# Kernel tuning notes

Hardware: AMD Instinct MI355X
Metric: run time of the kernel (lower is better)

Reference implementation:

```python
import jax, jax.numpy as jnp
import numpy as np

B, N, E = 8, 64, 192
D_IN, D_PROJ = 1024, 256
F = 16            # cfg.NGM.GNN_FEAT per layer
SK_TAU = 0.05     # cfg.NGM.SK_TAU
SK_ITERS = 10
BIN_ITERS = 10
NN = N * N


def _project(x, Wp, bp, gamma, beta):
    # self.projection: Linear(1024,256) -> BatchNorm1d(256) (batch stats) -> ReLU
    B_, M, _ = x.shape
    h = x.reshape(B_ * M, -1) @ Wp + bp
    mu = h.mean(0)
    var = h.var(0)
    h = (h - mu) / jnp.sqrt(var + 1e-5) * gamma + beta
    return jax.nn.relu(h).reshape(B_, M, -1)


def _l2n(x):
    return x / jnp.clip(jnp.linalg.norm(x, axis=-1, keepdims=True), 1e-12)


def _log_sinkhorn(log_s, iters):
    for _ in range(iters):
        log_s = log_s - jax.nn.logsumexp(log_s, axis=2, keepdims=True)
        log_s = log_s - jax.nn.logsumexp(log_s, axis=1, keepdims=True)
    return jnp.exp(log_s)


def _build_K(Ke, Kp, s1, d1, s2, d2):
    # construct_sparse_aff_mat: K[a2*N+a1, b2*N+b1] += Ke[e1, e2]
    rows = s2[None, :] * N + s1[:, None]      # [E, E]
    cols = d2[None, :] * N + d1[:, None]      # [E, E]
    flat = (rows.astype(jnp.int32) * NN + cols.astype(jnp.int32)).ravel()
    K = jnp.zeros((NN * NN,), Ke.dtype).at[flat].add(Ke.ravel()).reshape(NN, NN)
    diag = jnp.arange(NN)
    # diagonal holds vec(Kp^T) (ordering a2*N + a1, matching emb = Kp.T.reshape(-1,1))
    return K.at[diag, diag].set(Kp.T.ravel())


def setup_inputs() -> dict:
    key = jax.random.key(0)
    ks = jax.random.split(key, 32)
    inp = {}
    inp['x1'] = jax.random.normal(ks[0], (B, N, D_IN), jnp.float32)
    inp['x2'] = jax.random.normal(ks[1], (B, N, D_IN), jnp.float32)
    inp['e1'] = jax.random.normal(ks[2], (B, E, D_IN), jnp.float32)
    inp['e2'] = jax.random.normal(ks[3], (B, E, D_IN), jnp.float32)
    inp['Wp'] = jax.random.normal(ks[4], (D_IN, D_PROJ), jnp.float32) * 0.02
    inp['bp'] = jnp.zeros((D_PROJ,), jnp.float32)
    inp['gamma'] = jnp.ones((D_PROJ,), jnp.float32)
    inp['beta'] = jnp.zeros((D_PROJ,), jnp.float32)
    in_dims = [1, F + 1, F + 1]
    for i, din in enumerate(in_dims):
        inp[f'W{i}'] = jax.random.normal(ks[5 + 3 * i], (din, F), jnp.float32) * 0.2
        inp[f'b{i}'] = jnp.zeros((F,), jnp.float32)
        inp[f'S{i}'] = jax.random.normal(ks[6 + 3 * i], (F, 1), jnp.float32) * 0.2
        inp[f'c{i}'] = jnp.zeros((1,), jnp.float32)
    inp['Wc'] = jax.random.normal(ks[20], (F + 1, 1), jnp.float32) * 0.2
    inp['bc'] = jnp.zeros((1,), jnp.float32)
    inp['bin_value'] = jnp.ones((1,), jnp.float32) * 0.2
    inp['src1'] = jax.random.randint(ks[21], (B, E), 0, N, jnp.int32)
    inp['dst1'] = jax.random.randint(ks[22], (B, E), 0, N, jnp.int32)
    inp['src2'] = jax.random.randint(ks[23], (B, E), 0, N, jnp.int32)
    inp['dst2'] = jax.random.randint(ks[24], (B, E), 0, N, jnp.int32)
    return inp


def reference(x1, x2, e1, e2, Wp, bp, gamma, beta,
              W0, b0, S0, c0, W1, b1, S1, c1, W2, b2, S2, c2,
              Wc, bc, bin_value, src1, dst1, src2, dst2):
    # unary / quadratic affinities via projected, L2-normalized inner products
    p1 = _project(x1, Wp, bp, gamma, beta)
    p2 = _project(x2, Wp, bp, gamma, beta)
    q1 = _project(e1, Wp, bp, gamma, beta)
    q2 = _project(e2, Wp, bp, gamma, beta)
    Kp = jnp.einsum('bnd,bmd->bnm', _l2n(p1), _l2n(p2))        # [B, N1, N2]
    Ke = 0.5 * jnp.einsum('bed,bfd->bef', _l2n(q1), _l2n(q2))  # [B, E1, E2]
    # sparse Kronecker affinity assembled densely (association graph adjacency)
    K = jax.vmap(_build_K)(Ke, Kp, src1, dst1, src2, dst2)     # [B, NN, NN]
    A = (K > 0).astype(K.dtype)
    deg = jnp.clip(A.sum(-1), 1.0)                              # [B, NN]
    x = Kp.transpose(0, 2, 1).reshape(B, NN, 1)                 # emb = vec(Kp^T)
    for (W, b, S, c) in ((W0, b0, S0, c0), (W1, b1, S1, c1), (W2, b2, S2, c2)):
        msg = jnp.einsum('bij,bjc->bic', K, x) / deg[..., None]  # sparse matvec (memory-bound)
        h = jax.nn.relu(msg @ W + b)                             # [B, NN, F]
        v = (h @ S + c).reshape(B, N, N)                         # row order a2*N+a1 -> [B, N2, N1]
        ss = _log_sinkhorn(v.transpose(0, 2, 1) / SK_TAU, SK_ITERS)  # Sinkhorn embedding channel
        x = jnp.concatenate([h, ss.transpose(0, 2, 1).reshape(B, NN, 1)], -1)
    v = (x @ Wc + bc).reshape(B, N, N)
    s = v.transpose(0, 2, 1)                                    # [B, N1, N2]
    # BinSinkhorn: pad with learned bin value, dual normalization, strip bin
    binv = bin_value[0]
    ls = jnp.concatenate([s, jnp.full((B, 1, N), binv, s.dtype)], 1)
    ls = jnp.concatenate([ls, jnp.full((B, N + 1, 1), binv, s.dtype)], 2)
    P = _log_sinkhorn(ls, BIN_ITERS)
    ss = P[:, :N, :N]
    return ss / jax.lax.stop_gradient(ss.max())
```

## Files before the change

kernel.cpp:

```cpp
#include <hip/hip_runtime.h>

constexpr int kB   = 8;
constexpr int kN   = 64;
constexpr int kE   = 192;
constexpr int kDin = 1024;
constexpr int kDp  = 256;
constexpr int kNN  = 4096;
constexpr float kTauInv = 20.0f;
constexpr int kXS  = 16;
constexpr int kXP  = 18;

typedef float vfloat4 __attribute__((ext_vector_type(4)));

struct SmemGemm { float As[2][16][68]; float Ws[2][16][68]; };
struct SmemCsr  {
    int km1[4096], km2[4096];
    short es1[kE], es2[kE], rp1[kE], rp2[kE];
    int cnt1[64], cnt2[64], pos1[64], pos2[64];
    int ccnt1[kE], ccnt2[kE], cpos1[kE], cpos2[kE];
};
union __align__(16) SmemK1 { SmemGemm g; SmemCsr csr; };

__global__ __launch_bounds__(256) void k_projcsr(
    const float* __restrict__ x1, const float* __restrict__ x2,
    const float* __restrict__ e1, const float* __restrict__ e2,
    const float* __restrict__ Wp,
    const int* __restrict__ src1, const int* __restrict__ dst1,
    const int* __restrict__ src2, const int* __restrict__ dst2,
    float* __restrict__ P,
    int* __restrict__ off1, int* __restrict__ off2,
    int* __restrict__ lst1, int* __restrict__ lst2,
    int* __restrict__ rep1g, int* __restrict__ rep2g,
    int* __restrict__ coff1, int* __restrict__ coff2,
    int* __restrict__ clst1, int* __restrict__ clst2)
{
    const int bid = blockIdx.x, t = threadIdx.x;
    __shared__ SmemK1 u;

    if (bid < 512) {
        const int z = bid >> 8;
        const int rt = (bid >> 2) & 63, ct = bid & 3;
        const int grow0 = rt * 64, col0 = ct * 64;
        const float* src; int lrow0;
        if (rt < 8)       { src = x1; lrow0 = grow0; }
        else if (rt < 16) { src = x2; lrow0 = grow0 - 512; }
        else if (rt < 40) { src = e1; lrow0 = grow0 - 1024; }
        else              { src = e2; lrow0 = grow0 - 2560; }

        const int tx = t & 15, ty = t >> 4;
        const int arow = t >> 2, acol = (t & 3) * 4;
        const int wrow = t >> 4, wcol = (t & 15) * 4;

        const float* Abase = src + (size_t)(lrow0 + arow) * kDin + z * 512 + acol;
        const float* Wbase = Wp + (size_t)(z * 512 + wrow) * kDp + col0 + wcol;

        float4 a4 = *(const float4*)Abase;
        float4 w4 = *(const float4*)Wbase;
        float acc[4][4] = {};

        for (int c = 0; c < 32; ++c) {
            const int cur = c & 1;
            u.g.As[cur][acol + 0][arow] = a4.x;
            u.g.As[cur][acol + 1][arow] = a4.y;
            u.g.As[cur][acol + 2][arow] = a4.z;
            u.g.As[cur][acol + 3][arow] = a4.w;
            *(float4*)&u.g.Ws[cur][wrow][wcol] = w4;
            __syncthreads();
            if (c < 31) {
                a4 = *(const float4*)(Abase + (c + 1) * 16);
                w4 = *(const float4*)(Wbase + (size_t)(c + 1) * 16 * kDp);
            }
#pragma unroll
            for (int kk = 0; kk < 16; ++kk) {
                float4 av = *(const float4*)&u.g.As[cur][kk][ty * 4];
                float4 wv = *(const float4*)&u.g.Ws[cur][kk][tx * 4];
                float a[4] = {av.x, av.y, av.z, av.w};
                float w[4] = {wv.x, wv.y, wv.z, wv.w};
#pragma unroll
                for (int i = 0; i < 4; ++i)
#pragma unroll
                    for (int j = 0; j < 4; ++j)
                        acc[i][j] += a[i] * w[j];
            }
        }
        float* Pz = P + (size_t)z * 1048576;
#pragma unroll
        for (int i = 0; i < 4; ++i) {
            const int row = grow0 + ty * 4 + i;
            vfloat4 v;
            v.x = acc[i][0]; v.y = acc[i][1]; v.z = acc[i][2]; v.w = acc[i][3];
            __builtin_nontemporal_store(v, (vfloat4*)&Pz[(size_t)row * kDp + col0 + tx * 4]);
        }
    } else {
        const int b = bid - 512;
        auto& C = u.csr;
        for (int i = t; i < 4096; i += 256) {
            C.km1[i] = 0x7fffffff; C.km2[i] = 0x7fffffff;
        }
        if (t < 64) { C.cnt1[t] = 0; C.cnt2[t] = 0; }
        for (int i = t; i < kE; i += 256) { C.ccnt1[i] = 0; C.ccnt2[i] = 0; }
        __syncthreads();
        if (t < kE) {
            int v1 = src1[b * kE + t], v2 = src2[b * kE + t];
            C.es1[t] = (short)v1; C.es2[t] = (short)v2;
            atomicAdd(&C.cnt1[v1], 1);
            atomicAdd(&C.cnt2[v2], 1);
            atomicMin(&C.km1[v1 * 64 + dst1[b * kE + t]], t);
            atomicMin(&C.km2[v2 * 64 + dst2[b * kE + t]], t);
        }
        __syncthreads();
        if (t < kE) {
            int r1 = C.km1[C.es1[t] * 64 + dst1[b * kE + t]];
            int r2 = C.km2[C.es2[t] * 64 + dst2[b * kE + t]];
            C.rp1[t] = (short)r1; C.rp2[t] = (short)r2;
            rep1g[b * kE + t] = r1; rep2g[b * kE + t] = r2;
            atomicAdd(&C.ccnt1[r1], 1);
            atomicAdd(&C.ccnt2[r2], 1);
        }
        __syncthreads();
        if (t == 0) {
            int a = 0, c = 0;
            for (int v = 0; v < 64; ++v) { C.pos1[v] = a; a += C.cnt1[v]; C.pos2[v] = c; c += C.cnt2[v]; }
            a = 0; c = 0;
            for (int v = 0; v < kE; ++v) { C.cpos1[v] = a; a += C.ccnt1[v]; C.cpos2[v] = c; c += C.ccnt2[v]; }
        }
        __syncthreads();
        if (t < 64) { off1[b * 65 + t] = C.pos1[t]; off2[b * 65 + t] = C.pos2[t]; }
        if (t == 0) { off1[b * 65 + 64] = kE; off2[b * 65 + 64] = kE; }
        if (t < kE) { coff1[b * 193 + t] = C.cpos1[t]; coff2[b * 193 + t] = C.cpos2[t]; }
        if (t == 0) { coff1[b * 193 + kE] = kE; coff2[b * 193 + kE] = kE; }
        __syncthreads();
        if (t < kE) {
            int p = atomicAdd(&C.pos1[C.es1[t]], 1); lst1[b * kE + p] = t;
            int q = atomicAdd(&C.pos2[C.es2[t]], 1); lst2[b * kE + q] = t;
            int cp = atomicAdd(&C.cpos1[C.rp1[t]], 1); clst1[b * kE + cp] = t;
            int cq = atomicAdd(&C.cpos2[C.rp2[t]], 1); clst2[b * kE + cq] = t;
        }
    }
}

__global__ __launch_bounds__(256) void k_reduce(
    const float* __restrict__ P, const float* __restrict__ bp,
    float* __restrict__ hbuf, float* __restrict__ stats)
{
    const int t = threadIdx.x;
    const int r0 = blockIdx.x * 16;
    const int seg = (r0 < 512) ? 0 : (r0 < 1024 ? 1 : (r0 < 2560 ? 2 : 3));
    const float bb = bp[t];
    float s = 0.f, s2 = 0.f;
#pragma unroll
    for (int rr = 0; rr < 16; ++rr) {
        size_t o = (size_t)(r0 + rr) * kDp + t;
        float v = P[o] + P[o + 1048576] + bb;
        hbuf[o] = v;
        s += v; s2 += v * v;
    }
    atomicAdd(&stats[seg * 512 + t], s);
    atomicAdd(&stats[seg * 512 + 256 + t], s2);
}

struct __align__(16) SmemSim  {
    float Xs[32][36]; float Ys[32][36];
    float muX[256], isX[256], muY[256], isY[256];
    float ga[256], be[256];
    float scX[32], scY[32];
};

__global__ __launch_bounds__(256) void k_sim(
    const float* __restrict__ hbuf, const float* __restrict__ stats,
    const float* __restrict__ gamma, const float* __restrict__ beta,
    float* __restrict__ Kp, float* __restrict__ Ke)
{
    const int bid = blockIdx.x, t = threadIdx.x;
    __shared__ SmemSim u;

    const int id = bid % 40, b = bid / 40;
    int mt, nt_, ldo, segX, segY, xrow0, yrow0; float* outp; float scale;
    if (id < 4) {
        mt = (id >> 1) * 32; nt_ = (id & 1) * 32; ldo = 64;
        xrow0 = b * 64; yrow0 = 512 + b * 64;
        segX = 0; segY = 1;
        outp = Kp + (size_t)b * 4096; scale = 1.0f;
    } else {
        int e = id - 4;
        mt = (e / 6) * 32; nt_ = (e % 6) * 32; ldo = 192;
        xrow0 = 1024 + b * 192; yrow0 = 2560 + b * 192;
        segX = 2; segY = 3;
        outp = Ke + (size_t)b * 36864; scale = 0.5f;
    }
    {
        const float n = (segX < 2) ? 512.f : 1536.f;
        float mu = stats[segX * 512 + t] / n;
        float var = stats[segX * 512 + 256 + t] / n - mu * mu;
        u.muX[t] = mu; u.isX[t] = rsqrtf(var + 1e-5f);
        mu = stats[segY * 512 + t] / n;
        var = stats[segY * 512 + 256 + t] / n - mu * mu;
        u.muY[t] = mu; u.isY[t] = rsqrtf(var + 1e-5f);
        u.ga[t] = gamma[t]; u.be[t] = beta[t];
    }
    __syncthreads();
    {
        const int ri = t >> 2, lane = t & 3;
        const bool isXr = ri < 32;
        const int grow = isXr ? (xrow0 + mt + ri) : (yrow0 + nt_ + (ri - 32));
        const float* mus = isXr ? u.muX : u.muY;
        const float* iss = isXr ? u.isX : u.isY;
        const float* hr = hbuf + (size_t)grow * kDp;
        float ss = 0.f;
        for (int c4 = 0; c4 < 16; ++c4) {
            int c = lane * 64 + c4 * 4;
            float4 v = *(const float4*)&hr[c];
            float p;
            p = fmaxf((v.x - mus[c+0]) * iss[c+0] * u.ga[c+0] + u.be[c+0], 0.f); ss += p * p;
            p = fmaxf((v.y - mus[c+1]) * iss[c+1] * u.ga[c+1] + u.be[c+1], 0.f); ss += p * p;
            p = fmaxf((v.z - mus[c+2]) * iss[c+2] * u.ga[c+2] + u.be[c+2], 0.f); ss += p * p;
            p = fmaxf((v.w - mus[c+3]) * iss[c+3] * u.ga[c+3] + u.be[c+3], 0.f); ss += p * p;
        }
        ss += __shfl_xor(ss, 1);
        ss += __shfl_xor(ss, 2);
        if (lane == 0) {
            float sc = 1.f / fmaxf(sqrtf(ss), 1e-12f);
            if (isXr) u.scX[ri] = sc; else u.scY[ri - 32] = sc;
        }
    }
    __syncthreads();
    const int row = t >> 3, kq = t & 7;
    const int ty = t >> 4, tx = t & 15;
    const float* Xp = hbuf + (size_t)(xrow0 + mt) * kDp;
    const float* Yp = hbuf + (size_t)(yrow0 + nt_) * kDp;
    float acc[2][2] = {};
    for (int k0 = 0; k0 < kDp; k0 += 32) {
        const int c = k0 + kq * 4;
        float4 xa = *(const float4*)(Xp + (size_t)row * kDp + c);
        float4 ya = *(const float4*)(Yp + (size_t)row * kDp + c);
        const float sx = u.scX[row], sy = u.scY[row];
        u.Xs[kq*4+0][row] = fmaxf((xa.x - u.muX[c+0]) * u.isX[c+0] * u.ga[c+0] + u.be[c+0], 0.f) * sx;
        u.Xs[kq*4+1][row] = fmaxf((xa.y - u.muX[c+1]) * u.isX[c+1] * u.ga[c+1] + u.be[c+1], 0.f) * sx;
        u.Xs[kq*4+2][row] = fmaxf((xa.z - u.muX[c+2]) * u.isX[c+2] * u.ga[c+2] + u.be[c+2], 0.f) * sx;
        u.Xs[kq*4+3][row] = fmaxf((xa.w - u.muX[c+3]) * u.isX[c+3] * u.ga[c+3] + u.be[c+3], 0.f) * sx;
        u.Ys[kq*4+0][row] = fmaxf((ya.x - u.muY[c+0]) * u.isY[c+0] * u.ga[c+0] + u.be[c+0], 0.f) * sy;
        u.Ys[kq*4+1][row] = fmaxf((ya.y - u.muY[c+1]) * u.isY[c+1] * u.ga[c+1] + u.be[c+1], 0.f) * sy;
        u.Ys[kq*4+2][row] = fmaxf((ya.z - u.muY[c+2]) * u.isY[c+2] * u.ga[c+2] + u.be[c+2], 0.f) * sy;
        u.Ys[kq*4+3][row] = fmaxf((ya.w - u.muY[c+3]) * u.isY[c+3] * u.ga[c+3] + u.be[c+3], 0.f) * sy;
        __syncthreads();
#pragma unroll
        for (int kk = 0; kk < 32; ++kk) {
            float2 xv = *(const float2*)&u.Xs[kk][ty * 2];
            float2 yv = *(const float2*)&u.Ys[kk][tx * 2];
            acc[0][0] += xv.x * yv.x; acc[0][1] += xv.x * yv.y;
            acc[1][0] += xv.y * yv.x; acc[1][1] += xv.y * yv.y;
        }
        __syncthreads();
    }
#pragma unroll
    for (int i = 0; i < 2; ++i)
#pragma unroll
        for (int j = 0; j < 2; ++j)
            __builtin_nontemporal_store(scale * acc[i][j],
                &outp[(size_t)(mt + ty * 2 + i) * ldo + nt_ + tx * 2 + j]);
}

struct __align__(16) SmemLayer {
    float mat[64][68]; float fL[64], gL[64];
    float WL[17 * 16]; float bL[16], SL[16]; float c0v;
    float WcL[17];
    int jd2[kE]; int il[kE]; float msgT[64][18];
    int co1L[kE + 1], co2L[kE + 1];
    short cl1L[kE], cl2L[kE];
    float xs[64][kXP];
};

__device__ void sink64_local(int b, int t, float (*mat)[68], float* fL, float* gL,
                             const float* __restrict__ vin)
{
    const float4* v4 = (const float4*)(vin + b * kNN);
    for (int i = t; i < 1024; i += 256) {
        float4 v = v4[i];
        int idx = i * 4;
        int q = idx >> 6, p = idx & 63;
        mat[p][q]     = v.x * kTauInv;
        mat[p + 1][q] = v.y * kTauInv;
        mat[p + 2][q] = v.z * kTauInv;
        mat[p + 3][q] = v.w * kTauInv;
    }
    if (t < 64) { fL[t] = 0.f; gL[t] = 0.f; }
    __syncthreads();
    const int r = t >> 2, s = t & 3;
    float tv[16];
    for (int it = 0; it < 10; ++it) {
        float mx = -1e30f;
#pragma unroll
        for (int k = 0; k < 16; ++k) {
            float v = mat[r][s + 4 * k] + gL[s + 4 * k];
            tv[k] = v; mx = fmaxf(mx, v);
        }
        mx = fmaxf(mx, __shfl_xor(mx, 1));
        mx = fmaxf(mx, __shfl_xor(mx, 2));
        float sum = 0.f;
#pragma unroll
        for (int k = 0; k < 16; ++k) sum += __expf(tv[k] - mx);
        sum += __shfl_xor(sum, 1);
        sum += __shfl_xor(sum, 2);
        if (s == 0) fL[r] = -(mx + __logf(sum));
        __syncthreads();
        mx = -1e30f;
#pragma unroll
        for (int k = 0; k < 16; ++k) {
            float v = mat[s + 4 * k][r] + fL[s + 4 * k];
            tv[k] = v; mx = fmaxf(mx, v);
        }
        mx = fmaxf(mx, __shfl_xor(mx, 1));
        mx = fmaxf(mx, __shfl_xor(mx, 2));
        sum = 0.f;
#pragma unroll
        for (int k = 0; k < 16; ++k) sum += __expf(tv[k] - mx);
        sum += __shfl_xor(sum, 1);
        sum += __shfl_xor(sum, 2);
        if (s == 0) gL[r] = -(mx + __logf(sum));
        __syncthreads();
    }
    const float fr = fL[r];
#pragma unroll
    for (int k = 0; k < 16; ++k) {
        int q = s + 4 * k;
        mat[r][q] = __expf(mat[r][q] + fr + gL[q]);
    }
    __syncthreads();
}

template <int C, bool LASTP>
__device__ void layer_body(int bid, int t, SmemLayer& L,
    const int* __restrict__ off1, const int* __restrict__ lst1,
    const int* __restrict__ off2, const int* __restrict__ lst2,
    const int* __restrict__ d1, const int* __restrict__ d2,
    const int* __restrict__ rep1g, const int* __restrict__ rep2g,
    const int* __restrict__ coff1, const int* __restrict__ coff2,
    const int* __restrict__ clst1, const int* __restrict__ clst2,
    const float* __restrict__ Ke, const float* __restrict__ x,
    const float* __restrict__ Kp, int* __restrict__ degcnt,
    const float* __restrict__ W, const float* __restrict__ bb,
    const float* __restrict__ S, const float* __restrict__ c0,
    const float* __restrict__ Wc,
    const float* __restrict__ vprev, float* __restrict__ xn,
    float* __restrict__ vcbuf, float* __restrict__ vout)
{
    const int r2 = bid & 63, b = bid >> 6;
    for (int k = t; k < C * 16; k += 256) L.WL[k] = W[k];
    if (t < 16) { L.bL[t] = bb[t]; L.SL[t] = S[t]; }
    if (t == 0) L.c0v = c0[0];
    if (LASTP && t < 17) L.WcL[t] = Wc[t];
    const int j0 = off2[b * 65 + r2];
    const int n2 = off2[b * 65 + r2 + 1] - j0;
    for (int k = t; k < n2; k += 256) {
        int j = lst2[b * kE + j0 + k];
        int v = (j << 8) | d2[b * kE + j];
        if (C == 1 && rep2g[b * kE + j] == j) v |= 1 << 16;
        L.jd2[k] = v;
    }
    for (int k = t; k < kE; k += 256) {
        int i = lst1[b * kE + k];
        int v = (i << 8) | d1[b * kE + i];
        if (C == 1 && rep1g[b * kE + i] == i) v |= 1 << 16;
        L.il[k] = v;
    }
    if constexpr (C == 1) {
        for (int k = t; k < kE + 1; k += 256) {
            L.co1L[k] = coff1[b * 193 + k];
            L.co2L[k] = coff2[b * 193 + k];
        }
        for (int k = t; k < kE; k += 256) {
            L.cl1L[k] = (short)clst1[b * kE + k];
            L.cl2L[k] = (short)clst2[b * kE + k];
        }
    }
    if constexpr (C == 17) {
        sink64_local(b, t, L.mat, L.fL, L.gL, vprev);
    } else {
        __syncthreads();
    }

    const int r1 = t >> 2, lane = t & 3;
    const int i0 = off1[b * 65 + r1], i1 = off1[b * 65 + r1 + 1];
    const float* Keb = Ke + (size_t)b * kE * kE;
    const float* KpB = Kp + (size_t)b * kNN;
    int degLocal = 0;

    if constexpr (C == 1) {
        float acc = 0.f;
        for (int k = 0; k < n2; ++k) {
            int pk = L.jd2[k], j = (pk >> 8) & 255, dd2 = pk & 255;
            for (int m = i0 + lane; m < i1; m += 4) {
                int pi = L.il[m], i = (pi >> 8) & 255, dd1 = pi & 255;
                if (dd2 == r2 && dd1 == r1) continue;
                acc += Keb[(size_t)i * kE + j] * KpB[dd1 * 64 + dd2];
            }
        }
        acc += __shfl_xor(acc, 1);
        acc += __shfl_xor(acc, 2);
        if (lane == 0) L.msgT[r1][0] = acc;
        for (int m = i0 + lane; m < i1; m += 4) {
            int pi = L.il[m];
            if (!(pi >> 16)) continue;
            int i = (pi >> 8) & 255, dd1 = pi & 255;
            for (int k = 0; k < n2; ++k) {
                int pk = L.jd2[k];
                if (!(pk >> 16)) continue;
                int j = (pk >> 8) & 255, dd2 = pk & 255;
                float sum = 0.f;
                for (int mm = L.co1L[i]; mm < L.co1L[i + 1]; ++mm) {
                    const float* kr = Keb + (size_t)L.cl1L[mm] * kE;
                    for (int nn = L.co2L[j]; nn < L.co2L[j + 1]; ++nn)
                        sum += kr[L.cl2L[nn]];
                }
                if ((r2 * 64 + r1) != (dd2 * 64 + dd1) && sum > 0.0f) ++degLocal;
            }
        }
        degLocal += __shfl_xor(degLocal, 1);
        degLocal += __shfl_xor(degLocal, 2);
    } else {
        const float* xb = x + (size_t)b * kNN * kXS;
        float acc[5];
#pragma unroll
        for (int cc = 0; cc < 5; ++cc) acc[cc] = 0.f;
        for (int k = 0; k < n2; ++k) {
            int pk = L.jd2[k], j = (pk >> 8) & 255, dd2 = pk & 255;
            __syncthreads();
            {
                const float4* src4 = (const float4*)(xb + (size_t)(dd2 * 64) * kXS);
                float4 vv = src4[t];
                const int row = t >> 2, c4 = (t & 3) * 4;
                L.xs[row][c4 + 0] = vv.x; L.xs[row][c4 + 1] = vv.y;
                L.xs[row][c4 + 2] = vv.z; L.xs[row][c4 + 3] = vv.w;
            }
            __syncthreads();
            for (int m = i0; m < i1; ++m) {
                int pi = L.il[m], dd1 = pi & 255;
                if (dd2 == r2 && dd1 == r1) continue;
                int i = (pi >> 8) & 255;
                float kv = Keb[(size_t)i * kE + j];
                const float* xc = &L.xs[dd1][0];
                acc[0] += kv * xc[lane];
                acc[1] += kv * xc[lane + 4];
                acc[2] += kv * xc[lane + 8];
                acc[3] += kv * xc[lane + 12];
                if (lane == 0) acc[4] += kv * L.mat[dd1][dd2];
            }
        }
#pragma unroll
        for (int cc = 0; cc < 5; ++cc) {
            int c = lane + cc * 4;
            if (c < C) L.msgT[r1][c] = acc[cc];
        }
    }
    __syncthreads();

    const int row = r2 * 64 + r1;
    const int idx = b * kNN + row;
    const float kd = KpB[r1 * 64 + r2];
    int degv;
    if constexpr (C == 1) {
        degv = degLocal;
        if (lane == 0) __builtin_nontemporal_store(degLocal, &degcnt[idx]);
    } else {
        degv = degcnt[idx];
    }
    const float dg = fmaxf((float)(degv + (kd > 0.f ? 1 : 0)), 1.f);
    float m[C];
    if constexpr (C == 1) {
        m[0] = (L.msgT[r1][0] + kd * kd) / dg;
    } else {
        float4 xa  = *(const float4*)(x + (size_t)idx * kXS + 0);
        float4 xb4 = *(const float4*)(x + (size_t)idx * kXS + 4);
        float4 xc4 = *(const float4*)(x + (size_t)idx * kXS + 8);
        float4 xd4 = *(const float4*)(x + (size_t)idx * kXS + 12);
        m[0]  = (L.msgT[r1][0]  + kd * xa.x) / dg;
        m[1]  = (L.msgT[r1][1]  + kd * xa.y) / dg;
        m[2]  = (L.msgT[r1][2]  + kd * xa.z) / dg;
        m[3]  = (L.msgT[r1][3]  + kd * xa.w) / dg;
        m[4]  = (L.msgT[r1][4]  + kd * xb4.x) / dg;
        m[5]  = (L.msgT[r1][5]  + kd * xb4.y) / dg;
        m[6]  = (L.msgT[r1][6]  + kd * xb4.z) / dg;
        m[7]  = (L.msgT[r1][7]  + kd * xb4.w) / dg;
        m[8]  = (L.msgT[r1][8]  + kd * xc4.x) / dg;
        m[9]  = (L.msgT[r1][9]  + kd * xc4.y) / dg;
        m[10] = (L.msgT[r1][10] + kd * xc4.z) / dg;
        m[11] = (L.msgT[r1][11] + kd * xc4.w) / dg;
        m[12] = (L.msgT[r1][12] + kd * xd4.x) / dg;
        m[13] = (L.msgT[r1][13] + kd * xd4.y) / dg;
        m[14] = (L.msgT[r1][14] + kd * xd4.z) / dg;
        m[15] = (L.msgT[r1][15] + kd * xd4.w) / dg;
        m[16] = (L.msgT[r1][16] + kd * L.mat[r1][r2]) / dg;
    }
    float h[4];
    float vpart = 0.f;
#pragma unroll
    for (int ff = 0; ff < 4; ++ff) {
        int f = lane * 4 + ff;
        float a = L.bL[f];
#pragma unroll
        for (int c = 0; c < C; ++c) a += m[c] * L.WL[c * 16 + f];
        h[ff] = fmaxf(a, 0.f);
        vpart += h[ff] * L.SL[f];
    }
    if constexpr (!LASTP) {
        vfloat4 hv; hv.x = h[0]; hv.y = h[1]; hv.z = h[2]; hv.w = h[3];
        __builtin_nontemporal_store(hv, (vfloat4*)(xn + (size_t)idx * kXS + lane * 4));
    } else {
        float vcp = h[0] * L.WcL[lane * 4 + 0] + h[1] * L.WcL[lane * 4 + 1]
                  + h[2] * L.WcL[lane * 4 + 2] + h[3] * L.WcL[lane * 4 + 3];
        vcp += __shfl_xor(vcp, 1);
        vcp += __shfl_xor(vcp, 2);
        if (lane == 0) __builtin_nontemporal_store(vcp, &vcbuf[idx]);
    }
    vpart += __shfl_xor(vpart, 1);
    vpart += __shfl_xor(vpart, 2);
    if (lane == 0) __builtin_nontemporal_store(vpart + L.c0v, &vout[idx]);
}

__global__ __launch_bounds__(256) void k_l0(
    const int* __restrict__ off1, const int* __restrict__ lst1,
    const int* __restrict__ off2, const int* __restrict__ lst2,
    const int* __restrict__ dst1, const int* __restrict__ dst2,
    const int* __restrict__ rep1g, const int* __restrict__ rep2g,
    const int* __restrict__ coff1, const int* __restrict__ coff2,
    const int* __restrict__ clst1, const int* __restrict__ clst2,
    const float* __restrict__ Ke, const float* __restrict__ Kp,
    int* __restrict__ degcnt,
    const float* __restrict__ W0, const float* __restrict__ b0,
    const float* __restrict__ S0, const float* __restrict__ c0,
    float* __restrict__ xA, float* __restrict__ vA)
{
    __shared__ SmemLayer L;
    layer_body<1, false>(blockIdx.x, threadIdx.x, L,
        off1, lst1, off2, lst2, dst1, dst2, rep1g, rep2g,
        coff1, coff2, clst1, clst2, Ke, nullptr, Kp, degcnt,
        W0, b0, S0, c0, nullptr, nullptr, xA, nullptr, vA);
}

__global__ __launch_bounds__(256) void k_l1(
    const int* __restrict__ off1, const int* __restrict__ lst1,
    const int* __restrict__ off2, const int* __restrict__ lst2,
    const int* __restrict__ dst1, const int* __restrict__ dst2,
    const float* __restrict__ Ke, const float* __restrict__ Kp,
    int* __restrict__ degcnt,
    const float* __restrict__ W1, const float* __restrict__ b1,
    const float* __restrict__ S1, const float* __restrict__ c1,
    const float* __restrict__ xA, const float* __restrict__ vA,
    float* __restrict__ xB, float* __restrict__ vB)
{
    __shared__ SmemLayer L;
    layer_body<17, false>(blockIdx.x, threadIdx.x, L,
        off1, lst1, off2, lst2, dst1, dst2, nullptr, nullptr,
        nullptr, nullptr, nullptr, nullptr, Ke, xA, Kp, degcnt,
        W1, b1, S1, c1, nullptr, vA, xB, nullptr, vB);
}

__global__ __launch_bounds__(256) void k_l2(
    const int* __restrict__ off1, const int* __restrict__ lst1,
    const int* __restrict__ off2, const int* __restrict__ lst2,
    const int* __restrict__ dst1, const int* __restrict__ dst2,
    const float* __restrict__ Ke, const float* __restrict__ Kp,
    int* __restrict__ degcnt,
    const float* __restrict__ W2, const float* __restrict__ b2,
    const float* __restrict__ S2, const float* __restrict__ c2,
    const float* __restrict__ Wc,
    const float* __restrict__ xB, const float* __restrict__ vB,
    float* __restrict__ vcbuf, float* __restrict__ vA)
{
    __shared__ SmemLayer L;
    layer_body<17, true>(blockIdx.x, threadIdx.x, L,
        off1, lst1, off2, lst2, dst1, dst2, nullptr, nullptr,
        nullptr, nullptr, nullptr, nullptr, Ke, xB, Kp, degcnt,
        W2, b2, S2, c2, Wc, vB, nullptr, vcbuf, vA);
}

struct __align__(16) SmemSinkF {
    float mat[65][68]; float fL[72], gL[72];
    float wred[9];
};

__global__ __launch_bounds__(576) void k_final(
    const float* __restrict__ vA, const float* __restrict__ vcbuf,
    const float* __restrict__ Wc, const float* __restrict__ bc,
    const float* __restrict__ binv,
    int* __restrict__ bars, float* __restrict__ out)
{
    const int b = blockIdx.x, t = threadIdx.x;
    __shared__ SmemSinkF S;

    for (int i = t; i < kNN; i += 576) {
        int q = i >> 6, p = i & 63;
        S.mat[p][q] = vA[b * kNN + i] * kTauInv;
    }
    if (t < 72) { S.fL[t] = 0.f; S.gL[t] = 0.f; }
    __syncthreads();

    const int r = t >> 3, s = t & 7;

    {
        const bool act = r < 64;
        const int rr = act ? r : 0;
        float Lr[8], Lc[8], tv[8];
#pragma unroll
        for (int k = 0; k < 8; ++k) {
            Lr[k] = S.mat[rr][s + 8 * k];
            Lc[k] = S.mat[s + 8 * k][rr];
        }
        __syncthreads();
        for (int it = 0; it < 10; ++it) {
            float mx = -1e30f;
#pragma unroll
            for (int k = 0; k < 8; ++k) { tv[k] = Lr[k] + S.gL[s + 8 * k]; mx = fmaxf(mx, tv[k]); }
            mx = fmaxf(mx, __shfl_xor(mx, 1));
            mx = fmaxf(mx, __shfl_xor(mx, 2));
            mx = fmaxf(mx, __shfl_xor(mx, 4));
            float sum = 0.f;
#pragma unroll
            for (int k = 0; k < 8; ++k) sum += __expf(tv[k] - mx);
            sum += __shfl_xor(sum, 1);
            sum += __shfl_xor(sum, 2);
            sum += __shfl_xor(sum, 4);
            if (act && s == 0) S.fL[r] = -(mx + __logf(sum));
            __syncthreads();
            mx = -1e30f;
#pragma unroll
            for (int k = 0; k < 8; ++k) { tv[k] = Lc[k] + S.fL[s + 8 * k]; mx = fmaxf(mx, tv[k]); }
            mx = fmaxf(mx, __shfl_xor(mx, 1));
            mx = fmaxf(mx, __shfl_xor(mx, 2));
            mx = fmaxf(mx, __shfl_xor(mx, 4));
            sum = 0.f;
#pragma unroll
            for (int k = 0; k < 8; ++k) sum += __expf(tv[k] - mx);
            sum += __shfl_xor(sum, 1);
            sum += __shfl_xor(sum, 2);
            sum += __shfl_xor(sum, 4);
            if (act && s == 0) S.gL[r] = -(mx + __logf(sum));
            __syncthreads();
        }
        if (act) {
            const float fr = S.fL[r];
#pragma unroll
            for (int k = 0; k < 8; ++k) {
                int q = s + 8 * k;
                S.mat[r][q] = __expf(Lr[k] + fr + S.gL[q]);
            }
        }
    }
    __syncthreads();

    {
        const float Wc16 = Wc[16], bcv = bc[0], binvv = binv[0];
        const float* vcb = vcbuf + (size_t)b * kNN;
        for (int idx = t; idx < 65 * 65; idx += 576) {
            int q = idx / 65, p = idx - q * 65;
            float v;
            if (p < 64 && q < 64)
                v = vcb[q * 64 + p] + S.mat[p][q] * Wc16 + bcv;
            else v = binvv;
            S.mat[p][q] = v;
        }
        if (t < 72) { S.fL[t] = 0.f; S.gL[t] = 0.f; }
    }
    __syncthreads();

    const bool act = r < 65;
    const int rr = act ? r : 0;
    float Lrow[9], Lcol[9], tv[9];
#pragma unroll
    for (int k = 0; k < 8; ++k) {
        Lrow[k] = S.mat[rr][s + 8 * k];
        Lcol[k] = S.mat[s + 8 * k][rr];
    }
    Lrow[8] = (s == 0) ? S.mat[rr][64] : -1e30f;
    Lcol[8] = (s == 0) ? S.mat[64][rr] : -1e30f;
    __syncthreads();

    for (int it = 0; it < 10; ++it) {
        float mx = -1e30f;
#pragma unroll
        for (int k = 0; k < 9; ++k) { tv[k] = Lrow[k] + S.gL[s + 8 * k]; mx = fmaxf(mx, tv[k]); }
        mx = fmaxf(mx, __shfl_xor(mx, 1));
        mx = fmaxf(mx, __shfl_xor(mx, 2));
        mx = fmaxf(mx, __shfl_xor(mx, 4));
        float sum = 0.f;
#pragma unroll
        for (int k = 0; k < 9; ++k) sum += __expf(tv[k] - mx);
        sum += __shfl_xor(sum, 1);
        sum += __shfl_xor(sum, 2);
        sum += __shfl_xor(sum, 4);
        if (act && s == 0) S.fL[r] = -(mx + __logf(sum));
        __syncthreads();
        mx = -1e30f;
#pragma unroll
        for (int k = 0; k < 9; ++k) { tv[k] = Lcol[k] + S.fL[s + 8 * k]; mx = fmaxf(mx, tv[k]); }
        mx = fmaxf(mx, __shfl_xor(mx, 1));
        mx = fmaxf(mx, __shfl_xor(mx, 2));
        mx = fmaxf(mx, __shfl_xor(mx, 4));
        sum = 0.f;
#pragma unroll
        for (int k = 0; k < 9; ++k) sum += __expf(tv[k] - mx);
        sum += __shfl_xor(sum, 1);
        sum += __shfl_xor(sum, 2);
        sum += __shfl_xor(sum, 4);
        if (act && s == 0) S.gL[r] = -(mx + __logf(sum));
        __syncthreads();
    }

    float ev[8];
    float lmax = 0.f;
    if (r < 64) {
        const float fr = S.fL[r];
#pragma unroll
        for (int k = 0; k < 8; ++k) {
            ev[k] = __expf(Lrow[k] + fr + S.gL[s + 8 * k]);
            lmax = fmaxf(lmax, ev[k]);
        }
    }
#pragma unroll
    for (int o = 32; o >= 1; o >>= 1) lmax = fmaxf(lmax, __shfl_xor(lmax, o));
    if ((t & 63) == 0) S.wred[t >> 6] = lmax;
    __syncthreads();
    int* mcnt = bars + 3584;
    int* gmax = bars + 3600;
    if (t == 0) {
        float mb = S.wred[0];
#pragma unroll
        for (int w = 1; w < 9; ++w) mb = fmaxf(mb, S.wred[w]);
        atomicMax(gmax, __float_as_int(mb));
        asm volatile("s_waitcnt vmcnt(0)" ::: "memory");
        __hip_atomic_fetch_add(mcnt, 1, __ATOMIC_RELAXED, __HIP_MEMORY_SCOPE_AGENT);
        while (__hip_atomic_load(mcnt, __ATOMIC_RELAXED, __HIP_MEMORY_SCOPE_AGENT) < 8)
            __builtin_amdgcn_s_sleep(2);
    }
    __syncthreads();
    const float inv = 1.f / __int_as_float(
        __hip_atomic_load(gmax, __ATOMIC_RELAXED, __HIP_MEMORY_SCOPE_AGENT));
    if (r < 64) {
#pragma unroll
        for (int k = 0; k < 8; ++k)
            out[((size_t)b * kN + r) * kN + s + 8 * k] = ev[k] * inv;
    }
}

extern "C" void kernel_launch(void* const* d_in, const int* in_sizes, int n_in,
                              void* d_out, int out_size, void* d_ws, size_t ws_size,
                              hipStream_t stream)
{
    (void)in_sizes; (void)n_in; (void)out_size; (void)ws_size;

    const float* x1    = (const float*)d_in[0];
    const float* x2    = (const float*)d_in[1];
    const float* e1    = (const float*)d_in[2];
    const float* e2    = (const float*)d_in[3];
    const float* Wp    = (const float*)d_in[4];
    const float* bp    = (const float*)d_in[5];
    const float* gamma = (const float*)d_in[6];
    const float* beta  = (const float*)d_in[7];
    const float* W0 = (const float*)d_in[8];
    const float* b0 = (const float*)d_in[9];
    const float* S0 = (const float*)d_in[10];
    const float* c0 = (const float*)d_in[11];
    const float* W1 = (const float*)d_in[12];
    const float* b1 = (const float*)d_in[13];
    const float* S1 = (const float*)d_in[14];
    const float* c1 = (const float*)d_in[15];
    const float* W2 = (const float*)d_in[16];
    const float* b2 = (const float*)d_in[17];
    const float* S2 = (const float*)d_in[18];
    const float* c2 = (const float*)d_in[19];
    const float* Wc = (const float*)d_in[20];
    const float* bc = (const float*)d_in[21];
    const float* binv = (const float*)d_in[22];
    const int* src1 = (const int*)d_in[23];
    const int* dst1 = (const int*)d_in[24];
    const int* src2 = (const int*)d_in[25];
    const int* dst2 = (const int*)d_in[26];

    float* out = (float*)d_out;
    float* wsf = (float*)d_ws;

    float* hbuf  = wsf;
    float* P     = hbuf + 1048576;
    float* Kp    = P + 2097152;
    float* Ke    = Kp + 32768;
    float* vA    = Ke + 294912;
    float* vB    = vA + 32768;
    float* xA    = vB + 32768;
    float* xB    = xA + 524288;
    float* vcbuf = xB + 524288;
    int*   degcnt = (int*)(vcbuf + 32768);
    int*   off1 = degcnt + 32768;
    int*   off2 = off1 + 520;
    int*   lst1 = off2 + 520;
    int*   lst2 = lst1 + 1536;
    int*   rep1g = lst2 + 1536;
    int*   rep2g = rep1g + 1536;
    int*   coff1 = rep2g + 1536;
    int*   coff2 = coff1 + 1544;
    int*   clst1 = coff2 + 1544;
    int*   clst2 = clst1 + 1536;
    float* stats = (float*)(clst2 + 1536);
    int*   bars  = (int*)(stats + 2048);

    (void)hipMemsetAsync(stats, 0, (2048 + 4096) * sizeof(int), stream);
    k_projcsr<<<dim3(520), dim3(256), 0, stream>>>(
        x1, x2, e1, e2, Wp, src1, dst1, src2, dst2, P,
        off1, off2, lst1, lst2, rep1g, rep2g, coff1, coff2, clst1, clst2);
    k_reduce<<<dim3(256), dim3(256), 0, stream>>>(P, bp, hbuf, stats);
    k_sim<<<dim3(320), dim3(256), 0, stream>>>(hbuf, stats, gamma, beta, Kp, Ke);
    k_l0<<<dim3(512), dim3(256), 0, stream>>>(
        off1, lst1, off2, lst2, dst1, dst2, rep1g, rep2g,
        coff1, coff2, clst1, clst2, Ke, Kp, degcnt,
        W0, b0, S0, c0, xA, vA);
    k_l1<<<dim3(512), dim3(256), 0, stream>>>(
        off1, lst1, off2, lst2, dst1, dst2, Ke, Kp, degcnt,
        W1, b1, S1, c1, xA, vA, xB, vB);
    k_l2<<<dim3(512), dim3(256), 0, stream>>>(
        off1, lst1, off2, lst2, dst1, dst2, Ke, Kp, degcnt,
        W2, b2, S2, c2, Wc, xB, vB, vcbuf, vA);
    k_final<<<dim3(8), dim3(576), 0, stream>>>(vA, vcbuf, Wc, bc, binv, bars, out);
}
```

Measured before the change: 298.8 us.

## Hoist per-block redundant Sinkhorn into separate per-batch kernel

Before, every layer block (64 per batch) recomputed the full 64x64 Sinkhorn of the previous layer's scores in shared memory. The new code runs a dedicated k_sink kernel once per batch with 512 threads and register-cached rows and columns, writes the transposed result to global memory, and has layer blocks read only the column they need. Nontemporal stores are also replaced with plain stores. The cost is two extra launches with only 8 blocks each, which serialize on the stream.

```diff
diff --git a/kernel.cpp b/kernel.cpp
--- a/kernel.cpp
+++ b/kernel.cpp
@@ -87,9 +87,9 @@
 #pragma unroll
         for (int i = 0; i < 4; ++i) {
             const int row = grow0 + ty * 4 + i;
-            vfloat4 v;
+            float4 v;
             v.x = acc[i][0]; v.y = acc[i][1]; v.z = acc[i][2]; v.w = acc[i][3];
-            __builtin_nontemporal_store(v, (vfloat4*)&Pz[(size_t)row * kDp + col0 + tx * 4]);
+            *(float4*)&Pz[(size_t)row * kDp + col0 + tx * 4] = v;
         }
     } else {
         const int b = bid - 512;
@@ -256,25 +256,18 @@
     for (int i = 0; i < 2; ++i)
 #pragma unroll
         for (int j = 0; j < 2; ++j)
-            __builtin_nontemporal_store(scale * acc[i][j],
-                &outp[(size_t)(mt + ty * 2 + i) * ldo + nt_ + tx * 2 + j]);
-}
-
-struct __align__(16) SmemLayer {
-    float mat[64][68]; float fL[64], gL[64];
-    float WL[17 * 16]; float bL[16], SL[16]; float c0v;
-    float WcL[17];
-    int jd2[kE]; int il[kE]; float msgT[64][18];
-    int co1L[kE + 1], co2L[kE + 1];
-    short cl1L[kE], cl2L[kE];
-    float xs[64][kXP];
-};
-
-__device__ void sink64_local(int b, int t, float (*mat)[68], float* fL, float* gL,
-                             const float* __restrict__ vin)
-{
+            outp[(size_t)(mt + ty * 2 + i) * ldo + nt_ + tx * 2 + j] = scale * acc[i][j];
+}
+
+__global__ __launch_bounds__(512) void k_sink(
+    const float* __restrict__ vin, float* __restrict__ ssT)
+{
+    const int b = blockIdx.x, t = threadIdx.x;
+    __shared__ float mat[64][68];
+    __shared__ float fL[64], gL[64];
+
     const float4* v4 = (const float4*)(vin + b * kNN);
-    for (int i = t; i < 1024; i += 256) {
+    for (int i = t; i < 1024; i += 512) {
         float4 v = v4[i];
         int idx = i * 4;
         int q = idx >> 6, p = idx & 63;
@@ -285,48 +278,67 @@
     }
     if (t < 64) { fL[t] = 0.f; gL[t] = 0.f; }
     __syncthreads();
-    const int r = t >> 2, s = t & 3;
-    float tv[16];
+
+    const int r = t >> 3, s = t & 7;
+    float Lr[8], Lc[8], tv[8];
+#pragma unroll
+    for (int k = 0; k < 8; ++k) {
+        Lr[k] = mat[r][s + 8 * k];
+        Lc[k] = mat[s + 8 * k][r];
+    }
     for (int it = 0; it < 10; ++it) {
         float mx = -1e30f;
 #pragma unroll
-        for (int k = 0; k < 16; ++k) {
-            float v = mat[r][s + 4 * k] + gL[s + 4 * k];
-            tv[k] = v; mx = fmaxf(mx, v);
-        }
+        for (int k = 0; k < 8; ++k) { tv[k] = Lr[k] + gL[s + 8 * k]; mx = fmaxf(mx, tv[k]); }
         mx = fmaxf(mx, __shfl_xor(mx, 1));
         mx = fmaxf(mx, __shfl_xor(mx, 2));
+        mx = fmaxf(mx, __shfl_xor(mx, 4));
         float sum = 0.f;
 #pragma unroll
-        for (int k = 0; k < 16; ++k) sum += __expf(tv[k] - mx);
+        for (int k = 0; k < 8; ++k) sum += __expf(tv[k] - mx);
         sum += __shfl_xor(sum, 1);
         sum += __shfl_xor(sum, 2);
+        sum += __shfl_xor(sum, 4);
         if (s == 0) fL[r] = -(mx + __logf(sum));
         __syncthreads();
         mx = -1e30f;
 #pragma unroll
-        for (int k = 0; k < 16; ++k) {
-            float v = mat[s + 4 * k][r] + fL[s + 4 * k];
-            tv[k] = v; mx = fmaxf(mx, v);
-        }
+        for (int k = 0; k < 8; ++k) { tv[k] = Lc[k] + fL[s + 8 * k]; mx = fmaxf(mx, tv[k]); }
         mx = fmaxf(mx, __shfl_xor(mx, 1));
         mx = fmaxf(mx, __shfl_xor(mx, 2));
+        mx = fmaxf(mx, __shfl_xor(mx, 4));
         sum = 0.f;
 #pragma unroll
-        for (int k = 0; k < 16; ++k) sum += __expf(tv[k] - mx);
+        for (int k = 0; k < 8; ++k) sum += __expf(tv[k] - mx);
         sum += __shfl_xor(sum, 1);
         sum += __shfl_xor(sum, 2);
+        sum += __shfl_xor(sum, 4);
         if (s == 0) gL[r] = -(mx + __logf(sum));
         __syncthreads();
     }
     const float fr = fL[r];
 #pragma unroll
-    for (int k = 0; k < 16; ++k) {
-        int q = s + 4 * k;
-        mat[r][q] = __expf(mat[r][q] + fr + gL[q]);
-    }
-    __syncthreads();
-}
+    for (int k = 0; k < 8; ++k) {
+        int q = s + 8 * k;
+        mat[r][q] = __expf(Lr[k] + fr + gL[q]);
+    }
+    __syncthreads();
+    float* dst = ssT + (size_t)b * kNN;
+    for (int idx = t; idx < kNN; idx += 512) {
+        int q = idx >> 6, p = idx & 63;
+        dst[idx] = mat[p][q];
+    }
+}
+
+struct __align__(16) SmemLayer {
+    float WL[17 * 16]; float bL[16], SL[16]; float c0v;
+    float WcL[17];
+    int jd2[kE]; int il[kE]; float msgT[64][18];
+    int co1L[kE + 1], co2L[kE + 1];
+    short cl1L[kE], cl2L[kE];
+    float xs[64][kXP];
+    float sscol[64];
+};
 
 template <int C, bool LASTP>
 __device__ void layer_body(int bid, int t, SmemLayer& L,
@@ -341,7 +353,7 @@
     const float* __restrict__ W, const float* __restrict__ bb,
     const float* __restrict__ S, const float* __restrict__ c0,
     const float* __restrict__ Wc,
-    const float* __restrict__ vprev, float* __restrict__ xn,
+    const float* __restrict__ ssT, float* __restrict__ xn,
     float* __restrict__ vcbuf, float* __restrict__ vout)
 {
     const int r2 = bid & 63, b = bid >> 6;
@@ -373,16 +385,13 @@
             L.cl2L[k] = (short)clst2[b * kE + k];
         }
     }
-    if constexpr (C == 17) {
-        sink64_local(b, t, L.mat, L.fL, L.gL, vprev);
-    } else {
-        __syncthreads();
-    }
+    __syncthreads();
 
     const int r1 = t >> 2, lane = t & 3;
     const int i0 = off1[b * 65 + r1], i1 = off1[b * 65 + r1 + 1];
     const float* Keb = Ke + (size_t)b * kE * kE;
     const float* KpB = Kp + (size_t)b * kNN;
+    const float* ssTb = (C == 17) ? (ssT + (size_t)b * kNN) : nullptr;
     int degLocal = 0;
 
     if constexpr (C == 1) {
@@ -431,6 +440,8 @@
                 const int row = t >> 2, c4 = (t & 3) * 4;
                 L.xs[row][c4 + 0] = vv.x; L.xs[row][c4 + 1] = vv.y;
                 L.xs[row][c4 + 2] = vv.z; L.xs[row][c4 + 3] = vv.w;
+                if (t < 16)
+                    ((float4*)L.sscol)[t] = ((const float4*)(ssTb + dd2 * 64))[t];
             }
             __syncthreads();
             for (int m = i0; m < i1; ++m) {
@@ -443,7 +454,7 @@
                 acc[1] += kv * xc[lane + 4];
                 acc[2] += kv * xc[lane + 8];
                 acc[3] += kv * xc[lane + 12];
-                if (lane == 0) acc[4] += kv * L.mat[dd1][dd2];
+                if (lane == 0) acc[4] += kv * L.sscol[dd1];
             }
         }
 #pragma unroll
@@ -460,7 +471,7 @@
     int degv;
     if constexpr (C == 1) {
         degv = degLocal;
-        if (lane == 0) __builtin_nontemporal_store(degLocal, &degcnt[idx]);
+        if (lane == 0) degcnt[idx] = degLocal;
     } else {
         degv = degcnt[idx];
     }
@@ -489,7 +500,7 @@
         m[13] = (L.msgT[r1][13] + kd * xd4.y) / dg;
         m[14] = (L.msgT[r1][14] + kd * xd4.z) / dg;
         m[15] = (L.msgT[r1][15] + kd * xd4.w) / dg;
-        m[16] = (L.msgT[r1][16] + kd * L.mat[r1][r2]) / dg;
+        m[16] = (L.msgT[r1][16] + kd * ssTb[r2 * 64 + r1]) / dg;
     }
     float h[4];
     float vpart = 0.f;
@@ -503,18 +514,18 @@
         vpart += h[ff] * L.SL[f];
     }
     if constexpr (!LASTP) {
-        vfloat4 hv; hv.x = h[0]; hv.y = h[1]; hv.z = h[2]; hv.w = h[3];
-        __builtin_nontemporal_store(hv, (vfloat4*)(xn + (size_t)idx * kXS + lane * 4));
+        float4 hv; hv.x = h[0]; hv.y = h[1]; hv.z = h[2]; hv.w = h[3];
+        *(float4*)(xn + (size_t)idx * kXS + lane * 4) = hv;
     } else {
         float vcp = h[0] * L.WcL[lane * 4 + 0] + h[1] * L.WcL[lane * 4 + 1]
                   + h[2] * L.WcL[lane * 4 + 2] + h[3] * L.WcL[lane * 4 + 3];
         vcp += __shfl_xor(vcp, 1);
         vcp += __shfl_xor(vcp, 2);
-        if (lane == 0) __builtin_nontemporal_store(vcp, &vcbuf[idx]);
+        if (lane == 0) vcbuf[idx] = vcp;
     }
     vpart += __shfl_xor(vpart, 1);
     vpart += __shfl_xor(vpart, 2);
-    if (lane == 0) __builtin_nontemporal_store(vpart + L.c0v, &vout[idx]);
+    if (lane == 0) vout[idx] = vpart + L.c0v;
 }
 
 __global__ __launch_bounds__(256) void k_l0(
@@ -545,14 +556,14 @@
     int* __restrict__ degcnt,
     const float* __restrict__ W1, const float* __restrict__ b1,
     const float* __restrict__ S1, const float* __restrict__ c1,
-    const float* __restrict__ xA, const float* __restrict__ vA,
+    const float* __restrict__ xA, const float* __restrict__ ss,
     float* __restrict__ xB, float* __restrict__ vB)
 {
     __shared__ SmemLayer L;
     layer_body<17, false>(blockIdx.x, threadIdx.x, L,
         off1, lst1, off2, lst2, dst1, dst2, nullptr, nullptr,
         nullptr, nullptr, nullptr, nullptr, Ke, xA, Kp, degcnt,
-        W1, b1, S1, c1, nullptr, vA, xB, nullptr, vB);
+        W1, b1, S1, c1, nullptr, ss, xB, nullptr, vB);
 }
 
 __global__ __launch_bounds__(256) void k_l2(
@@ -564,14 +575,14 @@
     const float* __restrict__ W2, const float* __restrict__ b2,
     const float* __restrict__ S2, const float* __restrict__ c2,
     const float* __restrict__ Wc,
-    const float* __restrict__ xB, const float* __restrict__ vB,
+    const float* __restrict__ xB, const float* __restrict__ ss,
     float* __restrict__ vcbuf, float* __restrict__ vA)
 {
     __shared__ SmemLayer L;
     layer_body<17, true>(blockIdx.x, threadIdx.x, L,
         off1, lst1, off2, lst2, dst1, dst2, nullptr, nullptr,
         nullptr, nullptr, nullptr, nullptr, Ke, xB, Kp, degcnt,
-        W2, b2, S2, c2, Wc, vB, nullptr, vcbuf, vA);
+        W2, b2, S2, c2, Wc, ss, nullptr, vcbuf, vA);
 }
 
 struct __align__(16) SmemSinkF {
@@ -785,7 +796,8 @@
     float* Ke    = Kp + 32768;
     float* vA    = Ke + 294912;
     float* vB    = vA + 32768;
-    float* xA    = vB + 32768;
+    float* ss    = vB + 32768;
+    float* xA    = ss + 32768;
     float* xB    = xA + 524288;
     float* vcbuf = xB + 524288;
     int*   degcnt = (int*)(vcbuf + 32768);
@@ -812,11 +824,13 @@
         off1, lst1, off2, lst2, dst1, dst2, rep1g, rep2g,
         coff1, coff2, clst1, clst2, Ke, Kp, degcnt,
         W0, b0, S0, c0, xA, vA);
+    k_sink<<<dim3(8), dim3(512), 0, stream>>>(vA, ss);
     k_l1<<<dim3(512), dim3(256), 0, stream>>>(
         off1, lst1, off2, lst2, dst1, dst2, Ke, Kp, degcnt,
-        W1, b1, S1, c1, xA, vA, xB, vB);
+        W1, b1, S1, c1, xA, ss, xB, vB);
+    k_sink<<<dim3(8), dim3(512), 0, stream>>>(vB, ss);
     k_l2<<<dim3(512), dim3(256), 0, stream>>>(
         off1, lst1, off2, lst2, dst1, dst2, Ke, Kp, degcnt,
-        W2, b2, S2, c2, Wc, xB, vB, vcbuf, vA);
+        W2, b2, S2, c2, Wc, xB, ss, vcbuf, vA);
     k_final<<<dim3(8), dim3(576), 0, stream>>>(vA, vcbuf, Wc, bc, binv, bars, out);
 }
```

Result: faster. 292.3 us (-2.2%).
